# Kernel tuning notes

Hardware: AMD Instinct MI355X
Metric: run time of the kernel (lower is better)

## Reference

```python
import jax, jax.numpy as jnp
import numpy as np

T, B, DIN, H, NQ = 128, 256, 1024, 1024, 8
QDIM = H            # qdim must equal hidden_dim for f*cx elementwise product
D = DIN + H         # concat([x, hx]) feature width


def _qembed(z, enc_w, wire_w, wire_b):
    """QuantumEmbedding: linear encoder then sequential per-wire tanh updates.
    z: [B, QDIM]; enc_w: [QDIM, QDIM]; wire_w: [NQ, QDIM]; wire_b: [NQ].
    Wire i reads the CURRENT z (wires 0..i-1 already updated) -> sequential."""
    z = z @ enc_w.T
    for i in range(wire_w.shape[0]):  # small fixed loop (n_qubits)
        z = z.at[:, i].set(jnp.tanh(z @ wire_w[i] + wire_b[i]))
    return z


def setup_inputs() -> dict:
    key = jax.random.key(0)
    ks = jax.random.split(key, 14)
    s = 0.02
    return {
        "inputs": jax.random.normal(ks[0], (T, B, DIN), jnp.float32),
        # proj_to_q: Linear(D, QDIM)
        "Wq": s * jax.random.normal(ks[1], (QDIM, D), jnp.float32),
        "bq": jnp.zeros((QDIM,), jnp.float32),
        # forget quantum gate
        "enc_f": s * jax.random.normal(ks[2], (QDIM, QDIM), jnp.float32),
        "wf_w": s * jax.random.normal(ks[3], (NQ, QDIM), jnp.float32),
        "wf_b": jnp.zeros((NQ,), jnp.float32),
        # input quantum gate
        "enc_i": s * jax.random.normal(ks[4], (QDIM, QDIM), jnp.float32),
        "wi_w": s * jax.random.normal(ks[5], (NQ, QDIM), jnp.float32),
        "wi_b": jnp.zeros((NQ,), jnp.float32),
        # classical update gate: Linear(D, H)
        "Wu": s * jax.random.normal(ks[6], (H, D), jnp.float32),
        "bu": jnp.zeros((H,), jnp.float32),
        # classical output gate: Linear(D, H)
        "Wo": s * jax.random.normal(ks[7], (H, D), jnp.float32),
        "bo": jnp.zeros((H,), jnp.float32),
    }


def reference(inputs, Wq, bq, enc_f, wf_w, wf_b, enc_i, wi_w, wi_b, Wu, bu, Wo, bo):
    t, b, _ = inputs.shape
    h = Wu.shape[0]
    h0 = jnp.zeros((b, h), inputs.dtype)
    c0 = jnp.zeros((b, h), inputs.dtype)

    def step(carry, x):
        hx, cx = carry
        comb = jnp.concatenate([x, hx], axis=1)          # [B, D]
        zq = comb @ Wq.T + bq                            # [B, QDIM]
        f = jax.nn.sigmoid(_qembed(zq, enc_f, wf_w, wf_b))
        i = jax.nn.sigmoid(_qembed(zq, enc_i, wi_w, wi_b))
        g = jnp.tanh(comb @ Wu.T + bu)
        o = jax.nn.sigmoid(comb @ Wo.T + bo)
        cx = f * cx + i * g
        hx = o * jnp.tanh(cx)
        return (hx, cx), hx

    (hx, cx), outs = jax.lax.scan(step, (h0, c0), inputs)
    return outs, hx, cx
```

## Files before the change

### kernel.cpp

```cpp
#include <hip/hip_runtime.h>
#include <hip/hip_bf16.h>
#include <stdint.h>


#define T_STEPS 128
#define BATCH   256
#define DIN_    1024
#define HID_    1024
#define NQ_     8
#define DCAT    2048
#define NG      4096

using short8 = __attribute__((ext_vector_type(8))) short;
using f32x4  = __attribute__((ext_vector_type(4))) float;

static __device__ __forceinline__ ushort f2bf(float f) {
    union { float f; uint32_t u; } c{f};
    uint32_t u = c.u;
    uint32_t r = (u + 0x7fffu + ((u >> 16) & 1u)) >> 16;
    return (ushort)r;
}
static __device__ __forceinline__ float sigmoid_fast(float x) {
    return 1.f / (1.f + __expf(-x));
}
static __device__ __forceinline__ float tanh_fast(float x) {
    float xc = fminf(fmaxf(x, -15.f), 15.f);
    float e  = __expf(-2.f * xc);
    return (1.f - e) / (1.f + e);
}
static __device__ __forceinline__ void gload_lds16(const ushort* g, ushort* l) {
    __builtin_amdgcn_global_load_lds(
        (const __attribute__((address_space(1))) void*)g,
        (__attribute__((address_space(3))) void*)l, 16, 0, 0);
}


__global__ void quant_bf16_k(const float* __restrict__ src, ushort* __restrict__ dst, int n4) {
    int i = blockIdx.x * blockDim.x + threadIdx.x;
    if (i < n4) {
        float4 v = ((const float4*)src)[i];
        ushort4 o;
        o.x = f2bf(v.x); o.y = f2bf(v.y); o.z = f2bf(v.z); o.w = f2bf(v.w);
        ((ushort4*)dst)[i] = o;
    }
}

__global__ void transpose_quant_k(const float* __restrict__ Wq, ushort* __restrict__ WqT) {
    __shared__ float tile[32][33];
    int bx = blockIdx.x, by = blockIdx.y;
    int tx = threadIdx.x, ty = threadIdx.y;
#pragma unroll
    for (int p = 0; p < 4; ++p)
        tile[ty + 8*p][tx] = Wq[(size_t)(by*32 + ty + 8*p) * 2048 + bx*32 + tx];
    __syncthreads();
#pragma unroll
    for (int p = 0; p < 4; ++p)
        WqT[(size_t)(bx*32 + ty + 8*p) * 1024 + by*32 + tx] = f2bf(tile[tx][ty + 8*p]);
}

__global__ void bias_merge_k(const float* __restrict__ enc, const float* __restrict__ bq,
                             float* __restrict__ out) {
    int j = blockIdx.x * blockDim.x + threadIdx.x;
    const float* row = enc + (size_t)j * 1024;
    float s = 0.f;
    for (int m = 0; m < 1024; m += 4) {
        float4 e = *(const float4*)(row + m);
        float4 b = *(const float4*)(bq + m);
        s += e.x*b.x + e.y*b.y + e.z*b.z + e.w*b.w;
    }
    out[j] = s;
}

__global__ __launch_bounds__(256) void gemm_bt_ww_k(const ushort* __restrict__ A,
                                                    const ushort* __restrict__ Bt,
                                                    ushort* __restrict__ C,
                                                    int M, int N, int K) {
    __shared__ ushort As[64][72];
    __shared__ ushort Bs[64][72];
    const int tid = threadIdx.x;
    const int tile_n = blockIdx.x * 64;
    const int tile_m = blockIdx.y * 64;
    const int r8 = tid >> 3;
    const int c8 = (tid & 7) << 3;
    const int wid = tid >> 6, lane = tid & 63;
    const int wm = (wid >> 1) * 32, wn = (wid & 1) * 32;
    const int l15 = lane & 15, lk = (lane >> 4) << 3;

    f32x4 acc00 = {0,0,0,0}, acc01 = {0,0,0,0}, acc10 = {0,0,0,0}, acc11 = {0,0,0,0};

    for (int k0 = 0; k0 < K; k0 += 64) {
#pragma unroll
        for (int p = 0; p < 2; ++p) {
            int row = p*32 + r8;
            *(short8*)&As[row][c8] = *(const short8*)(A  + (size_t)(tile_m + row)*K + k0 + c8);
            *(short8*)&Bs[row][c8] = *(const short8*)(Bt + (size_t)(tile_n + row)*K + k0 + c8);
        }
        __syncthreads();
#pragma unroll
        for (int ks = 0; ks < 2; ++ks) {
            short8 a0 = *(short8*)&As[wm      + l15][ks*32 + lk];
            short8 a1 = *(short8*)&As[wm + 16 + l15][ks*32 + lk];
            short8 b0 = *(short8*)&Bs[wn      + l15][ks*32 + lk];
            short8 b1 = *(short8*)&Bs[wn + 16 + l15][ks*32 + lk];
            acc00 = __builtin_amdgcn_mfma_f32_16x16x32_bf16(a0, b0, acc00, 0, 0, 0);
            acc01 = __builtin_amdgcn_mfma_f32_16x16x32_bf16(a0, b1, acc01, 0, 0, 0);
            acc10 = __builtin_amdgcn_mfma_f32_16x16x32_bf16(a1, b0, acc10, 0, 0, 0);
            acc11 = __builtin_amdgcn_mfma_f32_16x16x32_bf16(a1, b1, acc11, 0, 0, 0);
        }
        __syncthreads();
    }
    const int orow = (lane >> 4) * 4;
#pragma unroll
    for (int r = 0; r < 4; ++r) {
        int m0 = tile_m + wm + orow + r;
        int n0 = tile_n + wn + l15;
        C[(size_t)m0*N + n0]           = f2bf(acc00[r]);
        C[(size_t)m0*N + n0 + 16]      = f2bf(acc01[r]);
        C[(size_t)(m0+16)*N + n0]      = f2bf(acc10[r]);
        C[(size_t)(m0+16)*N + n0 + 16] = f2bf(acc11[r]);
    }
}

__global__ __launch_bounds__(256, 2) void step_gemm2_k(
        const ushort* __restrict__ xbf, const ushort* __restrict__ hxb,
        const ushort* __restrict__ Wall,
        float* __restrict__ pre0, float* __restrict__ pre1, int t) {
    __shared__ ushort smem[2][8192];

    const int tid = threadIdx.x;
    const int wv = tid >> 6, ln = tid & 63;
    const int l15 = ln & 15, hk = ln >> 4;
    const int tile_n = blockIdx.x * 64;
    const int tile_m = blockIdx.y * 64;
    const int kh = blockIdx.z;

    const ushort* Asrc = kh ? (hxb + (size_t)tile_m * 1024)
                            : (xbf + ((size_t)t * BATCH + tile_m) * 1024);
    const ushort* Bsrc = Wall + (size_t)tile_n * DCAT + kh * 1024;
    float* pre = kh ? pre1 : pre0;

    const int wm = (wv >> 1) * 32, wn = (wv & 1) * 32;

    f32x4 acc[2][2] = {{{0,0,0,0},{0,0,0,0}},{{0,0,0,0},{0,0,0,0}}};

    const int srow = ln >> 3;
    const int scol = (ln & 7) * 8;
    const int scs  = scol ^ (srow << 3);

#define STAGE(BUFI, IT)                                                          \
    do {                                                                         \
        const int kof_ = (IT) * 64;                                              \
        _Pragma("unroll")                                                        \
        for (int j = 0; j < 4; ++j) {                                            \
            const int c_ = j * 4 + wv;                                           \
            const int r_ = (c_ & 7) * 8 + srow;                                  \
            const ushort* src_ = (c_ < 8)                                        \
                ? Asrc + (size_t)r_ * 1024 + kof_ + scs                          \
                : Bsrc + (size_t)r_ * 2048 + kof_ + scs;                         \
            gload_lds16(src_, &smem[BUFI][c_ * 512]);                            \
        }                                                                        \
    } while (0)

    STAGE(0, 0);
    asm volatile("s_waitcnt vmcnt(0)" ::: "memory");
    __builtin_amdgcn_s_barrier();

    int cur = 0;
#pragma unroll 1
    for (int it = 0; it < 16; ++it) {
        if (it + 1 < 16) STAGE(cur ^ 1, it + 1);

        const ushort* buf = smem[cur];
        short8 a[2][2], b[2][2];
#pragma unroll
        for (int ks = 0; ks < 2; ++ks) {
            const int kc = ks * 32 + hk * 8;
#pragma unroll
            for (int mi = 0; mi < 2; ++mi) {
                const int r = wm + mi * 16 + l15;
                a[mi][ks] = *(const short8*)&buf[r * 64 + (kc ^ ((r & 7) << 3))];
            }
#pragma unroll
            for (int ni = 0; ni < 2; ++ni) {
                const int r = wn + ni * 16 + l15;
                b[ni][ks] = *(const short8*)&buf[4096 + r * 64 + (kc ^ ((r & 7) << 3))];
            }
        }
#pragma unroll
        for (int ks = 0; ks < 2; ++ks)
#pragma unroll
            for (int mi = 0; mi < 2; ++mi)
#pragma unroll
                for (int ni = 0; ni < 2; ++ni)
                    acc[mi][ni] = __builtin_amdgcn_mfma_f32_16x16x32_bf16(
                        a[mi][ks], b[ni][ks], acc[mi][ni], 0, 0, 0);

        asm volatile("s_waitcnt vmcnt(0)" ::: "memory");
        __builtin_amdgcn_s_barrier();
        cur ^= 1;
    }
#undef STAGE

    const int orow = hk * 4;
#pragma unroll
    for (int mi = 0; mi < 2; ++mi)
#pragma unroll
        for (int ni = 0; ni < 2; ++ni)
#pragma unroll
            for (int r = 0; r < 4; ++r) {
                int m = tile_m + wm + mi * 16 + orow + r;
                int n = tile_n + wn + ni * 16 + l15;
                pre[(size_t)m * NG + n] = acc[mi][ni][r];
            }
}

__global__ __launch_bounds__(256) void step_pointwise2_k(
        const float* __restrict__ pre0, const float* __restrict__ pre1,
        const float* __restrict__ wfw, const float* __restrict__ wfb,
        const float* __restrict__ wiw, const float* __restrict__ wib,
        const float* __restrict__ bu,  const float* __restrict__ bo,
        const float* __restrict__ bias_zf, const float* __restrict__ bias_zi,
        float* __restrict__ cx, ushort* __restrict__ hxb,
        float* __restrict__ dout, int t) {
    __shared__ float zbuf[2][1024];
    __shared__ float gbuf[1024];
    __shared__ float obuf[1024];
    const int b = blockIdx.x;
    const int tid = threadIdx.x;
    const int wv = tid >> 6, ln = tid & 63;

    const float* p0 = pre0 + (size_t)b * NG;
    const float* p1 = pre1 + (size_t)b * NG;

    if (wv < 2) {
        const float* bias = wv ? bias_zi : bias_zf;
        const float* ww   = wv ? wiw : wfw;
        const float* wb   = wv ? wib : wfb;
        const int off = wv * 1024;
        float z[16];
#pragma unroll
        for (int j = 0; j < 16; ++j) {
            int k = j * 64 + ln;
            z[j] = p0[off + k] + p1[off + k] + bias[k];
        }
#pragma unroll
        for (int w = 0; w < NQ_; ++w) {
            float p = 0.f;
#pragma unroll
            for (int j = 0; j < 16; ++j) p += z[j] * ww[(size_t)w * 1024 + j * 64 + ln];
#pragma unroll
            for (int o = 1; o < 64; o <<= 1) p += __shfl_xor(p, o, 64);
            float s = tanh_fast(p + wb[w]);
            if (ln == w) z[0] = s;
        }
#pragma unroll
        for (int j = 0; j < 16; ++j) zbuf[wv][j * 64 + ln] = z[j];
    } else if (wv == 2) {
#pragma unroll
        for (int j = 0; j < 16; ++j) {
            int k = j * 64 + ln;
            gbuf[k] = tanh_fast(p0[2048 + k] + p1[2048 + k] + bu[k]);
        }
    } else {
#pragma unroll
        for (int j = 0; j < 16; ++j) {
            int k = j * 64 + ln;
            obuf[k] = sigmoid_fast(p0[3072 + k] + p1[3072 + k] + bo[k]);
        }
    }
    __syncthreads();

    float* cxr = cx + (size_t)b * HID_;
#pragma unroll
    for (int e = 0; e < 4; ++e) {
        int k = e * 256 + tid;
        float f = sigmoid_fast(zbuf[0][k]);
        float i = sigmoid_fast(zbuf[1][k]);
        float c = f * cxr[k] + i * gbuf[k];
        cxr[k] = c;
        float h = obuf[k] * tanh_fast(c);
        dout[(size_t)t * BATCH * HID_ + (size_t)b * HID_ + k] = h;
        hxb[(size_t)b * HID_ + k] = f2bf(h);
        if (t == T_STEPS - 1) {
            dout[(size_t)T_STEPS * BATCH * HID_ + (size_t)b * HID_ + k] = h;
            dout[(size_t)T_STEPS * BATCH * HID_ + (size_t)BATCH * HID_ + (size_t)b * HID_ + k] = c;
        }
    }
}

extern "C" void kernel_launch(void* const* d_in, const int* in_sizes, int n_in,
                              void* d_out, int out_size, void* d_ws, size_t ws_size,
                              hipStream_t stream) {
    const float* inputs = (const float*)d_in[0];
    const float* Wq     = (const float*)d_in[1];
    const float* bq     = (const float*)d_in[2];
    const float* enc_f  = (const float*)d_in[3];
    const float* wf_w   = (const float*)d_in[4];
    const float* wf_b   = (const float*)d_in[5];
    const float* enc_i  = (const float*)d_in[6];
    const float* wi_w   = (const float*)d_in[7];
    const float* wi_b   = (const float*)d_in[8];
    const float* Wu     = (const float*)d_in[9];
    const float* bu     = (const float*)d_in[10];
    const float* Wo     = (const float*)d_in[11];
    const float* bo     = (const float*)d_in[12];
    float* out = (float*)d_out;

    char* ws = (char*)d_ws;
    ushort* Wall    = (ushort*)(ws);
    ushort* xbf     = (ushort*)(ws + (16u<<20));
    float*  pre0    = (float*) (ws + (80u<<20));
    float*  pre1    = (float*) (ws + (84u<<20));
    float*  cx      = (float*) (ws + (88u<<20));
    ushort* hxb     = (ushort*)(ws + (89u<<20));
    float*  bias_zf = (float*) (ws + (89u<<20) + (512u<<10));
    float*  bias_zi = (float*) (ws + (89u<<20) + (512u<<10) + 4096);
    ushort* WqT     = (ushort*)(ws + (80u<<20));
    ushort* encfb   = (ushort*)(ws + (84u<<20));
    ushort* encib   = (ushort*)(ws + (86u<<20));

    hipMemsetAsync(cx,  0, (size_t)BATCH*HID_*sizeof(float), stream);
    hipMemsetAsync(hxb, 0, (size_t)BATCH*HID_*sizeof(ushort), stream);

    quant_bf16_k<<<1024, 256, 0, stream>>>(enc_f, encfb, 1024*1024/4);
    quant_bf16_k<<<1024, 256, 0, stream>>>(enc_i, encib, 1024*1024/4);
    quant_bf16_k<<<2048, 256, 0, stream>>>(Wu, Wall + (size_t)2048*DCAT, 1024*2048/4);
    quant_bf16_k<<<2048, 256, 0, stream>>>(Wo, Wall + (size_t)3072*DCAT, 1024*2048/4);
    transpose_quant_k<<<dim3(64, 32), dim3(32, 8), 0, stream>>>(Wq, WqT);
    bias_merge_k<<<4, 256, 0, stream>>>(enc_f, bq, bias_zf);
    bias_merge_k<<<4, 256, 0, stream>>>(enc_i, bq, bias_zi);
    gemm_bt_ww_k<<<dim3(32, 16), 256, 0, stream>>>(encfb, WqT, Wall, 1024, 2048, 1024);
    gemm_bt_ww_k<<<dim3(32, 16), 256, 0, stream>>>(encib, WqT, Wall + (size_t)1024*DCAT, 1024, 2048, 1024);

    quant_bf16_k<<<32768, 256, 0, stream>>>(inputs, xbf, T_STEPS*BATCH*DIN_/4);

    for (int t = 0; t < T_STEPS; ++t) {
        step_gemm2_k<<<dim3(64, 4, 2), 256, 0, stream>>>(xbf, hxb, Wall, pre0, pre1, t);
        step_pointwise2_k<<<256, 256, 0, stream>>>(
            pre0, pre1, wf_w, wf_b, wi_w, wi_b, bu, bo, bias_zf, bias_zi,
            cx, hxb, out, t);
    }
}
```

Measured before the change: 6.733 ms.

## Fuse per-step GEMM and pointwise into one persistent cooperative kernel

```diff
diff --git a/kernel.cpp b/kernel.cpp
--- a/kernel.cpp
+++ b/kernel.cpp
@@ -1,6 +1,9 @@
 #include <hip/hip_runtime.h>
 #include <hip/hip_bf16.h>
+#include <hip/hip_cooperative_groups.h>
 #include <stdint.h>
+
+namespace cg = cooperative_groups;
 
 
 #define T_STEPS 128
@@ -121,6 +124,7 @@
     }
 }
 
+
 __global__ __launch_bounds__(256, 2) void step_gemm2_k(
         const ushort* __restrict__ xbf, const ushort* __restrict__ hxb,
         const ushort* __restrict__ Wall,
@@ -144,8 +148,7 @@
     f32x4 acc[2][2] = {{{0,0,0,0},{0,0,0,0}},{{0,0,0,0},{0,0,0,0}}};
 
     const int srow = ln >> 3;
-    const int scol = (ln & 7) * 8;
-    const int scs  = scol ^ (srow << 3);
+    const int scs  = ((ln & 7) * 8) ^ (srow << 3);
 
 #define STAGE(BUFI, IT)                                                          \
     do {                                                                         \
@@ -285,6 +288,183 @@
             dout[(size_t)T_STEPS * BATCH * HID_ + (size_t)b * HID_ + k] = h;
             dout[(size_t)T_STEPS * BATCH * HID_ + (size_t)BATCH * HID_ + (size_t)b * HID_ + k] = c;
         }
+    }
+}
+
+__global__ __launch_bounds__(256, 2) void qlstm_persist_k(
+        const ushort* __restrict__ xbf, const ushort* __restrict__ Wall,
+        const float* __restrict__ wfw, const float* __restrict__ wfb,
+        const float* __restrict__ wiw, const float* __restrict__ wib,
+        const float* __restrict__ bu,  const float* __restrict__ bo,
+        const float* __restrict__ bias_zf, const float* __restrict__ bias_zi,
+        float* __restrict__ pre0, float* __restrict__ pre1,
+        float* __restrict__ cx, ushort* __restrict__ hxb,
+        float* __restrict__ dout) {
+    cg::grid_group grid = cg::this_grid();
+    __shared__ ushort smem[2][8192];
+
+    const int blk = blockIdx.x;
+    const int tid = threadIdx.x;
+    const int wv = tid >> 6, ln = tid & 63;
+    const int l15 = ln & 15, hk = ln >> 4;
+
+    const int kh = blk >> 8;
+    const int job = blk & 255;
+    const int tile_n = (job & 63) * 64;
+    const int tile_m = (job >> 6) * 64;
+    const ushort* Bsrc = Wall + (size_t)tile_n * DCAT + kh * 1024;
+    float* pre = kh ? pre1 : pre0;
+    const int wm = (wv >> 1) * 32, wn = (wv & 1) * 32;
+    const int srow = ln >> 3;
+    const int scs  = ((ln & 7) * 8) ^ (srow << 3);
+
+    float* zbuf = (float*)smem;
+    float* gbuf = (float*)smem + 2048;
+    float* obuf = (float*)smem + 3072;
+
+    for (int t = 0; t < T_STEPS; ++t) {
+        const ushort* Asrc = kh ? (hxb + (size_t)tile_m * 1024)
+                                : (xbf + ((size_t)t * BATCH + tile_m) * 1024);
+
+        f32x4 acc[2][2];
+#pragma unroll
+        for (int mi = 0; mi < 2; ++mi)
+#pragma unroll
+            for (int ni = 0; ni < 2; ++ni)
+                acc[mi][ni] = (f32x4){0.f, 0.f, 0.f, 0.f};
+
+#define STAGE(BUFI, IT)                                                          \
+    do {                                                                         \
+        const int kof_ = (IT) * 64;                                              \
+        _Pragma("unroll")                                                        \
+        for (int j = 0; j < 4; ++j) {                                            \
+            const int c_ = j * 4 + wv;                                           \
+            const int r_ = (c_ & 7) * 8 + srow;                                  \
+            const ushort* src_ = (c_ < 8)                                        \
+                ? Asrc + (size_t)r_ * 1024 + kof_ + scs                          \
+                : Bsrc + (size_t)r_ * 2048 + kof_ + scs;                         \
+            gload_lds16(src_, &smem[BUFI][c_ * 512]);                            \
+        }                                                                        \
+    } while (0)
+
+        STAGE(0, 0);
+        STAGE(1, 1);
+        asm volatile("s_waitcnt vmcnt(4)" ::: "memory");
+        __builtin_amdgcn_s_barrier();
+
+#pragma unroll 1
+        for (int it = 0; it < 16; ++it) {
+            const ushort* buf = smem[it & 1];
+            short8 a[2][2], b[2][2];
+#pragma unroll
+            for (int ks = 0; ks < 2; ++ks) {
+                const int kc = ks * 32 + hk * 8;
+#pragma unroll
+                for (int mi = 0; mi < 2; ++mi) {
+                    const int r = wm + mi * 16 + l15;
+                    a[mi][ks] = *(const short8*)&buf[r * 64 + (kc ^ ((r & 7) << 3))];
+                }
+#pragma unroll
+                for (int ni = 0; ni < 2; ++ni) {
+                    const int r = wn + ni * 16 + l15;
+                    b[ni][ks] = *(const short8*)&buf[4096 + r * 64 + (kc ^ ((r & 7) << 3))];
+                }
+            }
+#pragma unroll
+            for (int ks = 0; ks < 2; ++ks)
+#pragma unroll
+                for (int mi = 0; mi < 2; ++mi)
+#pragma unroll
+                    for (int ni = 0; ni < 2; ++ni)
+                        acc[mi][ni] = __builtin_amdgcn_mfma_f32_16x16x32_bf16(
+                            a[mi][ks], b[ni][ks], acc[mi][ni], 0, 0, 0);
+
+            __builtin_amdgcn_s_barrier();
+            if (it + 2 < 16) STAGE(it & 1, it + 2);
+            if (it + 1 < 16) {
+                if (it + 2 < 16) asm volatile("s_waitcnt vmcnt(4)" ::: "memory");
+                else             asm volatile("s_waitcnt vmcnt(0)" ::: "memory");
+                __builtin_amdgcn_s_barrier();
+            }
+        }
+#undef STAGE
+
+        {
+            const int orow = hk * 4;
+#pragma unroll
+            for (int mi = 0; mi < 2; ++mi)
+#pragma unroll
+                for (int ni = 0; ni < 2; ++ni)
+#pragma unroll
+                    for (int r = 0; r < 4; ++r) {
+                        int m = tile_m + wm + mi * 16 + orow + r;
+                        int n = tile_n + wn + ni * 16 + l15;
+                        pre[(size_t)m * NG + n] = acc[mi][ni][r];
+                    }
+        }
+        grid.sync();
+
+        if (blk < BATCH) {
+            const int b = blk;
+            const float* p0 = pre0 + (size_t)b * NG;
+            const float* p1 = pre1 + (size_t)b * NG;
+
+            if (wv < 2) {
+                const float* bias = wv ? bias_zi : bias_zf;
+                const float* ww   = wv ? wiw : wfw;
+                const float* wb   = wv ? wib : wfb;
+                const int off = wv * 1024;
+                float z[16];
+#pragma unroll
+                for (int j = 0; j < 16; ++j) {
+                    int k = j * 64 + ln;
+                    z[j] = p0[off + k] + p1[off + k] + bias[k];
+                }
+#pragma unroll
+                for (int w = 0; w < NQ_; ++w) {
+                    float p = 0.f;
+#pragma unroll
+                    for (int j = 0; j < 16; ++j) p += z[j] * ww[(size_t)w * 1024 + j * 64 + ln];
+#pragma unroll
+                    for (int o = 1; o < 64; o <<= 1) p += __shfl_xor(p, o, 64);
+                    float s = tanh_fast(p + wb[w]);
+                    if (ln == w) z[0] = s;
+                }
+#pragma unroll
+                for (int j = 0; j < 16; ++j) zbuf[wv * 1024 + j * 64 + ln] = z[j];
+            } else if (wv == 2) {
+#pragma unroll
+                for (int j = 0; j < 16; ++j) {
+                    int k = j * 64 + ln;
+                    gbuf[k] = tanh_fast(p0[2048 + k] + p1[2048 + k] + bu[k]);
+                }
+            } else {
+#pragma unroll
+                for (int j = 0; j < 16; ++j) {
+                    int k = j * 64 + ln;
+                    obuf[k] = sigmoid_fast(p0[3072 + k] + p1[3072 + k] + bo[k]);
+                }
+            }
+            __syncthreads();
+
+            float* cxr = cx + (size_t)b * HID_;
+#pragma unroll
+            for (int e = 0; e < 4; ++e) {
+                int k = e * 256 + tid;
+                float f = sigmoid_fast(zbuf[k]);
+                float i = sigmoid_fast(zbuf[1024 + k]);
+                float c = f * cxr[k] + i * gbuf[k];
+                cxr[k] = c;
+                float h = obuf[k] * tanh_fast(c);
+                dout[(size_t)t * BATCH * HID_ + (size_t)b * HID_ + k] = h;
+                hxb[(size_t)b * HID_ + k] = f2bf(h);
+                if (t == T_STEPS - 1) {
+                    dout[(size_t)T_STEPS * BATCH * HID_ + (size_t)b * HID_ + k] = h;
+                    dout[(size_t)T_STEPS * BATCH * HID_ + (size_t)BATCH * HID_ + (size_t)b * HID_ + k] = c;
+                }
+            }
+        }
+        grid.sync();
     }
 }
 
@@ -334,10 +514,20 @@
 
     quant_bf16_k<<<32768, 256, 0, stream>>>(inputs, xbf, T_STEPS*BATCH*DIN_/4);
 
-    for (int t = 0; t < T_STEPS; ++t) {
-        step_gemm2_k<<<dim3(64, 4, 2), 256, 0, stream>>>(xbf, hxb, Wall, pre0, pre1, t);
-        step_pointwise2_k<<<256, 256, 0, stream>>>(
-            pre0, pre1, wf_w, wf_b, wi_w, wi_b, bu, bo, bias_zf, bias_zi,
-            cx, hxb, out, t);
-    }
-}
+    void* args[] = {
+        (void*)&xbf, (void*)&Wall,
+        (void*)&wf_w, (void*)&wf_b, (void*)&wi_w, (void*)&wi_b,
+        (void*)&bu, (void*)&bo, (void*)&bias_zf, (void*)&bias_zi,
+        (void*)&pre0, (void*)&pre1, (void*)&cx, (void*)&hxb, (void*)&out
+    };
+    hipError_t rc = hipLaunchCooperativeKernel((void*)qlstm_persist_k,
+                                               dim3(512), dim3(256), args, 0, stream);
+    if (rc != hipSuccess) {
+        for (int t = 0; t < T_STEPS; ++t) {
+            step_gemm2_k<<<dim3(64, 4, 2), 256, 0, stream>>>(xbf, hxb, Wall, pre0, pre1, t);
+            step_pointwise2_k<<<256, 256, 0, stream>>>(
+                pre0, pre1, wf_w, wf_b, wi_w, wi_b, bu, bo, bias_zf, bias_zi,
+                cx, hxb, out, t);
+        }
+    }
+}
```

Result: slower. 21.58 ms (+220.5%).
